# Performance work log

Measured on AMD Instinct MI355X. Metric: run time of the kernel, lower is better.

Reference implementation:

```python
import jax, jax.numpy as jnp
import numpy as np


def _layernorm(x, g, b, eps=1e-5):
    mu = x.mean(-1, keepdims=True)
    var = ((x - mu) ** 2).mean(-1, keepdims=True)
    return (x - mu) / jnp.sqrt(var + eps) * g + b


def _bilinear_sample(feat, coords):
    # feat: (B,C,H,W,D); coords: (B,C,N,2) normalized to [-1,1]
    # torch.grid_sample(mode='bilinear', padding_mode='zeros', align_corners=True)
    B, C, H, W, D = feat.shape
    x = (coords[..., 0] + 1.0) * 0.5 * (W - 1)  # grid x -> width axis
    y = (coords[..., 1] + 1.0) * 0.5 * (H - 1)  # grid y -> height axis
    x0 = jnp.floor(x)
    y0 = jnp.floor(y)
    wx1 = x - x0
    wy1 = y - y0
    bi = jnp.arange(B)[:, None, None]
    ci = jnp.arange(C)[None, :, None]

    def corner(yi, xi, w):
        inb = (xi >= 0) & (xi < W) & (yi >= 0) & (yi < H)
        xc = jnp.clip(xi, 0, W - 1).astype(jnp.int32)
        yc = jnp.clip(yi, 0, H - 1).astype(jnp.int32)
        v = feat[bi, ci, yc, xc]  # (B,C,N,D) gather
        return v * (w * inb)[..., None]

    return (corner(y0, x0, (1 - wy1) * (1 - wx1))
            + corner(y0, x0 + 1, (1 - wy1) * wx1)
            + corner(y0 + 1, x0, wy1 * (1 - wx1))
            + corner(y0 + 1, x0 + 1, wy1 * wx1))


def setup_inputs() -> dict:
    key = jax.random.key(0)
    ks = jax.random.split(key, 12)
    B, C, N, D, H, W = 2, 8, 16384, 256, 64, 64
    s = 1.0 / np.sqrt(D).astype(np.float32)
    return {
        "queries": jax.random.normal(ks[0], (B, N, D), jnp.float32),
        "image_features": jax.random.normal(ks[1], (B, C, H, W, D), jnp.float32),
        "pixel_coords": jax.random.uniform(ks[2], (B, C, N, 2), jnp.float32) * 2.0 - 1.0,
        "valid_mask": jax.random.randint(ks[3], (B, C, N), 0, 2).astype(jnp.int32),
        "Wq": jax.random.normal(ks[4], (D, D), jnp.float32) * s,
        "bq": jnp.zeros((D,), jnp.float32),
        "Wkv": jax.random.normal(ks[5], (D, 2 * D), jnp.float32) * s,
        "bkv": jnp.zeros((2 * D,), jnp.float32),
        "Wo": jax.random.normal(ks[6], (D, D), jnp.float32) * s,
        "bo": jnp.zeros((D,), jnp.float32),
        "gamma": jnp.ones((D,), jnp.float32),
        "beta": jnp.zeros((D,), jnp.float32),
    }


def reference(queries, image_features, pixel_coords, valid_mask,
              Wq, bq, Wkv, bkv, Wo, bo, gamma, beta):
    B, N, D = queries.shape
    residual = queries
    qn = _layernorm(queries, gamma, beta)
    sampled = _bilinear_sample(image_features, pixel_coords)      # (B,C,N,D)
    sampled = jnp.transpose(sampled, (0, 2, 1, 3))                 # (B,N,C,D)
    q = qn @ Wq + bq                                               # (B,N,D)
    kv = sampled @ Wkv + bkv                                       # (B,N,C,2D)
    k, v = kv[..., :D], kv[..., D:]
    scores = jnp.einsum('bnd,bncd->bnc', q, k) / jnp.sqrt(jnp.float32(D))
    valid = jnp.transpose(valid_mask, (0, 2, 1)) != 0              # (B,N,C)
    scores = jnp.where(valid, scores, -jnp.inf)
    attn = jax.nn.softmax(scores, axis=-1)
    attn = jnp.where(jnp.isnan(attn), 0.0, attn)                   # all-invalid -> 0
    out = jnp.einsum('bnc,bncd->bnd', attn, v)
    return residual + out @ Wo + bo
```

## Files before the change

### kernel.cpp

```cpp
#include <hip/hip_runtime.h>
#include <math.h>

#define NROWS 32768

typedef __attribute__((ext_vector_type(8))) short short8;
typedef __attribute__((ext_vector_type(4))) float f32x4;

#define WS_ABF    0
#define WS_WVOBF  32768
#define WS_PB     65536
#define WS_BVO    65792
#define WS_SUMA   66048
#define WS_P      98816
#define WS_FEATBF 8487424

__device__ __forceinline__ unsigned short f2bf(float f) {
    unsigned u = __builtin_bit_cast(unsigned, f);
    u += 0x7FFFu + ((u >> 16) & 1u);
    return (unsigned short)(u >> 16);
}
__device__ __forceinline__ float bf_lo(unsigned u) {
    return __builtin_bit_cast(float, u << 16);
}
__device__ __forceinline__ float bf_hi(unsigned u) {
    return __builtin_bit_cast(float, u & 0xFFFF0000u);
}

__global__ __launch_bounds__(256)
void precompute_kernel(const float* __restrict__ Wq, const float* __restrict__ bq,
                       const float* __restrict__ Wkv, const float* __restrict__ bkv,
                       const float* __restrict__ Wo, const float* __restrict__ feat,
                       float* __restrict__ ws) {
    int t = threadIdx.x;
    int blk = blockIdx.x;
    if (blk >= 514) {
        long i = (long)(blk - 514) * 1024 + t * 4;
        float4 v = *(const float4*)(feat + i);
        unsigned lo = (unsigned)f2bf(v.x) | ((unsigned)f2bf(v.y) << 16);
        unsigned hi = (unsigned)f2bf(v.z) | ((unsigned)f2bf(v.w) << 16);
        *(uint2*)((unsigned short*)(ws + WS_FEATBF) + i) = make_uint2(lo, hi);
        return;
    }
    if (blk < 256) {
        int f = blk;
        const float4* wq4 = (const float4*)(Wq + f * 256);
        const float4* wk4 = (const float4*)(Wkv + (long)t * 512);
        float acc = 0.f;
        #pragma unroll 8
        for (int d4 = 0; d4 < 64; ++d4) {
            float4 a = wq4[d4], b = wk4[d4];
            acc += a.x * b.x + a.y * b.y + a.z * b.z + a.w * b.w;
        }
        ((unsigned short*)(ws + WS_ABF))[t * 256 + f] = f2bf(acc);
    } else if (blk < 512) {
        int e = blk - 256;
        float acc = 0.f;
        for (int g = 0; g < 256; ++g)
            acc = fmaf(Wkv[(long)e * 512 + 256 + g], Wo[g * 256 + t], acc);
        ((unsigned short*)(ws + WS_WVOBF))[t * 256 + e] = f2bf(acc);
    } else if (blk == 512) {
        float acc = 0.f;
        for (int d = 0; d < 256; ++d)
            acc = fmaf(bq[d], Wkv[(long)t * 512 + d], acc);
        ws[WS_PB + t] = acc;
    } else {
        float acc = 0.f;
        for (int g = 0; g < 256; ++g)
            acc = fmaf(bkv[256 + g], Wo[g * 256 + t], acc);
        ws[WS_BVO + t] = acc;
    }
}

__global__ __launch_bounds__(256)
void ln_p_mfma(const float* __restrict__ queries, const float* __restrict__ gamma,
               const float* __restrict__ beta, float* __restrict__ ws) {
    __shared__ unsigned short qs[64][264];
    const unsigned short* Abf = (const unsigned short*)(ws + WS_ABF);
    const float* pb = ws + WS_PB;
    float* pbuf = ws + WS_P;
    int tid = threadIdx.x, wave = tid >> 6, lane = tid & 63;
    long row0 = (long)blockIdx.x * 64;

    float4 g4 = *(const float4*)(gamma + 4 * lane);
    float4 b4 = *(const float4*)(beta + 4 * lane);
    for (int rr = 0; rr < 16; ++rr) {
        int r = wave * 16 + rr;
        float4 v = *(const float4*)(queries + (row0 + r) * 256 + 4 * lane);
        float s = v.x + v.y + v.z + v.w;
        s += __shfl_xor(s, 32); s += __shfl_xor(s, 16); s += __shfl_xor(s, 8);
        s += __shfl_xor(s, 4);  s += __shfl_xor(s, 2);  s += __shfl_xor(s, 1);
        float mu = s * 0.00390625f;
        float dx = v.x - mu, dy = v.y - mu, dz = v.z - mu, dw = v.w - mu;
        float vv = dx * dx + dy * dy + dz * dz + dw * dw;
        vv += __shfl_xor(vv, 32); vv += __shfl_xor(vv, 16); vv += __shfl_xor(vv, 8);
        vv += __shfl_xor(vv, 4);  vv += __shfl_xor(vv, 2);  vv += __shfl_xor(vv, 1);
        float rstd = rsqrtf(vv * 0.00390625f + 1e-5f);
        float qx = dx * rstd * g4.x + b4.x;
        float qy = dy * rstd * g4.y + b4.y;
        float qz = dz * rstd * g4.z + b4.z;
        float qw = dw * rstd * g4.w + b4.w;
        unsigned lo = (unsigned)f2bf(qx) | ((unsigned)f2bf(qy) << 16);
        unsigned hi = (unsigned)f2bf(qz) | ((unsigned)f2bf(qw) << 16);
        *(uint2*)&qs[r][4 * lane] = make_uint2(lo, hi);
    }
    __syncthreads();

    int r16 = lane & 15, g = lane >> 4;
    f32x4 zero = {0.f, 0.f, 0.f, 0.f};
    f32x4 acc[4][4];
    #pragma unroll
    for (int mt = 0; mt < 4; ++mt)
        #pragma unroll
        for (int nt = 0; nt < 4; ++nt) acc[mt][nt] = zero;

    #pragma unroll
    for (int ks = 0; ks < 8; ++ks) {
        short8 bfr[4], afr[4];
        #pragma unroll
        for (int nt = 0; nt < 4; ++nt)
            bfr[nt] = *(const short8*)(Abf + ((wave * 64 + nt * 16 + r16) << 8) + ks * 32 + g * 8);
        #pragma unroll
        for (int mt = 0; mt < 4; ++mt)
            afr[mt] = *(const short8*)(&qs[mt * 16 + r16][ks * 32 + g * 8]);
        #pragma unroll
        for (int mt = 0; mt < 4; ++mt)
            #pragma unroll
            for (int nt = 0; nt < 4; ++nt)
                acc[mt][nt] = __builtin_amdgcn_mfma_f32_16x16x32_bf16(afr[mt], bfr[nt], acc[mt][nt], 0, 0, 0);
    }

    float pbv[4];
    #pragma unroll
    for (int nt = 0; nt < 4; ++nt) pbv[nt] = pb[wave * 64 + nt * 16 + r16];
    #pragma unroll
    for (int mt = 0; mt < 4; ++mt)
        #pragma unroll
        for (int nt = 0; nt < 4; ++nt)
            #pragma unroll
            for (int rg = 0; rg < 4; ++rg)
                pbuf[(row0 + mt * 16 + g * 4 + rg) * 256 + wave * 64 + nt * 16 + r16] =
                    acc[mt][nt][rg] + pbv[nt];
}

__global__ __launch_bounds__(256)
void sample_attn_bf(const float* __restrict__ coords, const int* __restrict__ vmask,
                    float* __restrict__ ws) {
    float* pbuf = ws + WS_P;
    float* suma = ws + WS_SUMA;
    const unsigned short* featbf = (const unsigned short*)(ws + WS_FEATBF);
    int tid = threadIdx.x, wave = tid >> 6, lane = tid & 63;
    long row = (long)blockIdx.x * 4 + wave;
    int b = (int)(row >> 14);
    int n = (int)(row & 16383);

    float4 p4 = *(const float4*)(pbuf + row * 256 + 4 * lane);

    float4 sc[8];
    float score[8];
    bool vld[8];
    #pragma unroll
    for (int c = 0; c < 8; ++c) {
        long cb = (long)(b * 8 + c) * 16384 + n;
        float cx = coords[2 * cb];
        float cy = coords[2 * cb + 1];
        vld[c] = (vmask[cb] != 0);
        float x = (cx + 1.f) * 31.5f;
        float y = (cy + 1.f) * 31.5f;
        float x0f = floorf(x), y0f = floorf(y);
        float wx = x - x0f, wy = y - y0f;
        int ix0 = (int)x0f, iy0 = (int)y0f;
        int ix1 = ix0 + 1, iy1 = iy0 + 1;
        float bx0 = (ix0 >= 0 && ix0 < 64) ? 1.f : 0.f;
        float bx1 = (ix1 >= 0 && ix1 < 64) ? 1.f : 0.f;
        float by0 = (iy0 >= 0 && iy0 < 64) ? 1.f : 0.f;
        float by1 = (iy1 >= 0 && iy1 < 64) ? 1.f : 0.f;
        int cx0 = min(max(ix0, 0), 63), cx1 = min(max(ix1, 0), 63);
        int cy0 = min(max(iy0, 0), 63), cy1 = min(max(iy1, 0), 63);
        const unsigned short* fb = featbf + ((long)(b * 8 + c) << 20);
        const uint2* r00 = (const uint2*)(fb + ((cy0 * 64 + cx0) << 8)) + lane;
        const uint2* r01 = (const uint2*)(fb + ((cy0 * 64 + cx1) << 8)) + lane;
        const uint2* r10 = (const uint2*)(fb + ((cy1 * 64 + cx0) << 8)) + lane;
        const uint2* r11 = (const uint2*)(fb + ((cy1 * 64 + cx1) << 8)) + lane;
        float w00 = (1.f - wy) * (1.f - wx) * by0 * bx0;
        float w01 = (1.f - wy) * wx * by0 * bx1;
        float w10 = wy * (1.f - wx) * by1 * bx0;
        float w11 = wy * wx * by1 * bx1;
        uint2 v00 = *r00, v01 = *r01, v10 = *r10, v11 = *r11;
        float4 s;
        s.x = w00 * bf_lo(v00.x) + w01 * bf_lo(v01.x) + w10 * bf_lo(v10.x) + w11 * bf_lo(v11.x);
        s.y = w00 * bf_hi(v00.x) + w01 * bf_hi(v01.x) + w10 * bf_hi(v10.x) + w11 * bf_hi(v11.x);
        s.z = w00 * bf_lo(v00.y) + w01 * bf_lo(v01.y) + w10 * bf_lo(v10.y) + w11 * bf_lo(v11.y);
        s.w = w00 * bf_hi(v00.y) + w01 * bf_hi(v01.y) + w10 * bf_hi(v10.y) + w11 * bf_hi(v11.y);
        sc[c] = s;
        float t = s.x * p4.x + s.y * p4.y + s.z * p4.z + s.w * p4.w;
        t += __shfl_xor(t, 32); t += __shfl_xor(t, 16); t += __shfl_xor(t, 8);
        t += __shfl_xor(t, 4);  t += __shfl_xor(t, 2);  t += __shfl_xor(t, 1);
        score[c] = t * 0.0625f;
    }

    float m = -INFINITY;
    #pragma unroll
    for (int c = 0; c < 8; ++c) if (vld[c]) m = fmaxf(m, score[c]);
    float4 sb = {0.f, 0.f, 0.f, 0.f};
    float sa = 0.f;
    if (m > -INFINITY) {
        float w[8], s = 0.f;
        #pragma unroll
        for (int c = 0; c < 8; ++c) { w[c] = vld[c] ? expf(score[c] - m) : 0.f; s += w[c]; }
        float inv = 1.f / s;
        #pragma unroll
        for (int c = 0; c < 8; ++c) {
            float a = w[c] * inv;
            sb.x = fmaf(a, sc[c].x, sb.x);
            sb.y = fmaf(a, sc[c].y, sb.y);
            sb.z = fmaf(a, sc[c].z, sb.z);
            sb.w = fmaf(a, sc[c].w, sb.w);
        }
        sa = 1.f;
    }
    unsigned lo = (unsigned)f2bf(sb.x) | ((unsigned)f2bf(sb.y) << 16);
    unsigned hi = (unsigned)f2bf(sb.z) | ((unsigned)f2bf(sb.w) << 16);
    ((uint2*)((char*)pbuf + row * 1024))[lane] = make_uint2(lo, hi);
    if (lane == 0) suma[row] = sa;
}

__global__ __launch_bounds__(256)
void final_mfma(const float* __restrict__ queries, const float* __restrict__ bo,
                const float* __restrict__ ws, float* __restrict__ out) {
    __shared__ unsigned short qs[64][264];
    __shared__ float ssu[64];
    const unsigned short* Wvobf = (const unsigned short*)(ws + WS_WVOBF);
    const float* bvo = ws + WS_BVO;
    const float* suma = ws + WS_SUMA;
    const float* pbuf = ws + WS_P;
    int tid = threadIdx.x, wave = tid >> 6, lane = tid & 63;
    long row0 = (long)blockIdx.x * 64;

    for (int rr = 0; rr < 16; ++rr) {
        int r = wave * 16 + rr;
        uint2 v = ((const uint2*)((const char*)pbuf + (row0 + r) * 1024))[lane];
        *(uint2*)&qs[r][4 * lane] = v;
    }
    if (tid < 64) ssu[tid] = suma[row0 + tid];
    __syncthreads();

    int r16 = lane & 15, g = lane >> 4;
    f32x4 zero = {0.f, 0.f, 0.f, 0.f};
    f32x4 acc[4][4];
    #pragma unroll
    for (int mt = 0; mt < 4; ++mt)
        #pragma unroll
        for (int nt = 0; nt < 4; ++nt) acc[mt][nt] = zero;

    #pragma unroll
    for (int ks = 0; ks < 8; ++ks) {
        short8 bfr[4], afr[4];
        #pragma unroll
        for (int nt = 0; nt < 4; ++nt)
            bfr[nt] = *(const short8*)(Wvobf + ((wave * 64 + nt * 16 + r16) << 8) + ks * 32 + g * 8);
        #pragma unroll
        for (int mt = 0; mt < 4; ++mt)
            afr[mt] = *(const short8*)(&qs[mt * 16 + r16][ks * 32 + g * 8]);
        #pragma unroll
        for (int mt = 0; mt < 4; ++mt)
            #pragma unroll
            for (int nt = 0; nt < 4; ++nt)
                acc[mt][nt] = __builtin_amdgcn_mfma_f32_16x16x32_bf16(afr[mt], bfr[nt], acc[mt][nt], 0, 0, 0);
    }

    float bvov[4], bov[4];
    #pragma unroll
    for (int nt = 0; nt < 4; ++nt) {
        int col = wave * 64 + nt * 16 + r16;
        bvov[nt] = bvo[col];
        bov[nt] = bo[col];
    }
    #pragma unroll
    for (int mt = 0; mt < 4; ++mt)
        #pragma unroll
        for (int nt = 0; nt < 4; ++nt)
            #pragma unroll
            for (int rg = 0; rg < 4; ++rg) {
                long row = row0 + mt * 16 + g * 4 + rg;
                int col = wave * 64 + nt * 16 + r16;
                out[row * 256 + col] = queries[row * 256 + col] + acc[mt][nt][rg]
                                     + ssu[mt * 16 + g * 4 + rg] * bvov[nt] + bov[nt];
            }
}

extern "C" void kernel_launch(void* const* d_in, const int* in_sizes, int n_in,
                              void* d_out, int out_size, void* d_ws, size_t ws_size,
                              hipStream_t stream) {
    const float* queries = (const float*)d_in[0];
    const float* feat    = (const float*)d_in[1];
    const float* coords  = (const float*)d_in[2];
    const int*   vmask   = (const int*)  d_in[3];
    const float* Wq      = (const float*)d_in[4];
    const float* bq      = (const float*)d_in[5];
    const float* Wkv     = (const float*)d_in[6];
    const float* bkv     = (const float*)d_in[7];
    const float* Wo      = (const float*)d_in[8];
    const float* bo      = (const float*)d_in[9];
    const float* gamma   = (const float*)d_in[10];
    const float* beta    = (const float*)d_in[11];
    float* out = (float*)d_out;
    float* ws  = (float*)d_ws;

    precompute_kernel<<<514 + 16384, 256, 0, stream>>>(Wq, bq, Wkv, bkv, Wo, feat, ws);
    ln_p_mfma<<<NROWS / 64, 256, 0, stream>>>(queries, gamma, beta, ws);
    sample_attn_bf<<<NROWS / 4, 256, 0, stream>>>(coords, vmask, ws);
    final_mfma<<<NROWS / 64, 256, 0, stream>>>(queries, bo, ws, out);
}
```

Measured before the change: 278.3 us.

## Store projected queries as bf16, pre-swizzle weights, process two rows per wave

The projected query buffer P is now written as bf16 with the 1/sqrt(D) scale folded in, staged through LDS so global stores are coalesced. This halves P traffic and shrinks the workspace. Weight matrices are stored in MFMA fragment order so each lane's B-fragment load is contiguous. The sampling kernel processes two rows per wave with 16-byte gathers, uses fast exp, and adds unroll pragmas to the small precompute loops. The cost is extra bf16 rounding on the query projection, plus more registers per thread in the sampling kernel.

Measured after the change: 363.9 us. +30.8%, slower.

```diff
diff --git a/kernel.cpp b/kernel.cpp
--- a/kernel.cpp
+++ b/kernel.cpp
@@ -7,12 +7,12 @@
 typedef __attribute__((ext_vector_type(4))) float f32x4;
 
 #define WS_ABF    0
-#define WS_WVOBF  32768
+#define WS_WVOF   32768
 #define WS_PB     65536
 #define WS_BVO    65792
 #define WS_SUMA   66048
 #define WS_P      98816
-#define WS_FEATBF 8487424
+#define WS_FEATBF 4293120
 
 __device__ __forceinline__ unsigned short f2bf(float f) {
     unsigned u = __builtin_bit_cast(unsigned, f);
@@ -24,6 +24,11 @@
 }
 __device__ __forceinline__ float bf_hi(unsigned u) {
     return __builtin_bit_cast(float, u & 0xFFFF0000u);
+}
+__device__ __forceinline__ int fragidx(int outcol, int k) {
+    int ct = outcol >> 4, r16 = outcol & 15;
+    int ks = k >> 5, g = (k >> 3) & 3, j = k & 7;
+    return ((((ct << 3) + ks) << 6) + (g << 4) + r16) * 8 + j;
 }
 
 __global__ __launch_bounds__(256)
@@ -51,20 +56,23 @@
             float4 a = wq4[d4], b = wk4[d4];
             acc += a.x * b.x + a.y * b.y + a.z * b.z + a.w * b.w;
         }
-        ((unsigned short*)(ws + WS_ABF))[t * 256 + f] = f2bf(acc);
+        ((unsigned short*)(ws + WS_ABF))[fragidx(t, f)] = f2bf(acc);
     } else if (blk < 512) {
         int e = blk - 256;
         float acc = 0.f;
+        #pragma unroll 8
         for (int g = 0; g < 256; ++g)
             acc = fmaf(Wkv[(long)e * 512 + 256 + g], Wo[g * 256 + t], acc);
-        ((unsigned short*)(ws + WS_WVOBF))[t * 256 + e] = f2bf(acc);
+        ((unsigned short*)(ws + WS_WVOF))[fragidx(t, e)] = f2bf(acc);
     } else if (blk == 512) {
         float acc = 0.f;
+        #pragma unroll 8
         for (int d = 0; d < 256; ++d)
             acc = fmaf(bq[d], Wkv[(long)t * 512 + d], acc);
         ws[WS_PB + t] = acc;
     } else {
         float acc = 0.f;
+        #pragma unroll 8
         for (int g = 0; g < 256; ++g)
             acc = fmaf(bkv[256 + g], Wo[g * 256 + t], acc);
         ws[WS_BVO + t] = acc;
@@ -75,9 +83,9 @@
 void ln_p_mfma(const float* __restrict__ queries, const float* __restrict__ gamma,
                const float* __restrict__ beta, float* __restrict__ ws) {
     __shared__ unsigned short qs[64][264];
-    const unsigned short* Abf = (const unsigned short*)(ws + WS_ABF);
+    const unsigned short* Afrag = (const unsigned short*)(ws + WS_ABF);
     const float* pb = ws + WS_PB;
-    float* pbuf = ws + WS_P;
+    unsigned short* pbf = (unsigned short*)(ws + WS_P);
     int tid = threadIdx.x, wave = tid >> 6, lane = tid & 63;
     long row0 = (long)blockIdx.x * 64;
 
@@ -118,7 +126,7 @@
         short8 bfr[4], afr[4];
         #pragma unroll
         for (int nt = 0; nt < 4; ++nt)
-            bfr[nt] = *(const short8*)(Abf + ((wave * 64 + nt * 16 + r16) << 8) + ks * 32 + g * 8);
+            bfr[nt] = *(const short8*)(Afrag + (((((wave * 4 + nt) << 3) + ks) << 6) + lane) * 8);
         #pragma unroll
         for (int mt = 0; mt < 4; ++mt)
             afr[mt] = *(const short8*)(&qs[mt * 16 + r16][ks * 32 + g * 8]);
@@ -128,6 +136,7 @@
             for (int nt = 0; nt < 4; ++nt)
                 acc[mt][nt] = __builtin_amdgcn_mfma_f32_16x16x32_bf16(afr[mt], bfr[nt], acc[mt][nt], 0, 0, 0);
     }
+    __syncthreads();
 
     float pbv[4];
     #pragma unroll
@@ -138,34 +147,46 @@
         for (int nt = 0; nt < 4; ++nt)
             #pragma unroll
             for (int rg = 0; rg < 4; ++rg)
-                pbuf[(row0 + mt * 16 + g * 4 + rg) * 256 + wave * 64 + nt * 16 + r16] =
-                    acc[mt][nt][rg] + pbv[nt];
+                qs[mt * 16 + g * 4 + rg][wave * 64 + nt * 16 + r16] =
+                    f2bf((acc[mt][nt][rg] + pbv[nt]) * 0.0625f);
+    __syncthreads();
+
+    for (int rr = 0; rr < 16; ++rr) {
+        int r = wave * 16 + rr;
+        uint2 v = *(const uint2*)&qs[r][4 * lane];
+        *(uint2*)(pbf + ((row0 + r) << 8) + 4 * lane) = v;
+    }
 }
 
 __global__ __launch_bounds__(256)
-void sample_attn_bf(const float* __restrict__ coords, const int* __restrict__ vmask,
-                    float* __restrict__ ws) {
-    float* pbuf = ws + WS_P;
+void sample_attn2(const float* __restrict__ coords, const int* __restrict__ vmask,
+                  float* __restrict__ ws) {
+    unsigned short* pbf = (unsigned short*)(ws + WS_P);
     float* suma = ws + WS_SUMA;
     const unsigned short* featbf = (const unsigned short*)(ws + WS_FEATBF);
     int tid = threadIdx.x, wave = tid >> 6, lane = tid & 63;
-    long row = (long)blockIdx.x * 4 + wave;
+    int h = lane >> 5, l5 = lane & 31;
+    long row = (long)blockIdx.x * 8 + wave * 2 + h;
     int b = (int)(row >> 14);
     int n = (int)(row & 16383);
 
-    float4 p4 = *(const float4*)(pbuf + row * 256 + 4 * lane);
-
-    float4 sc[8];
+    uint4 pv = *(const uint4*)(pbf + (row << 8) + (l5 << 3));
+    float p8[8];
+    p8[0] = bf_lo(pv.x); p8[1] = bf_hi(pv.x);
+    p8[2] = bf_lo(pv.y); p8[3] = bf_hi(pv.y);
+    p8[4] = bf_lo(pv.z); p8[5] = bf_hi(pv.z);
+    p8[6] = bf_lo(pv.w); p8[7] = bf_hi(pv.w);
+
+    float sc[8][8];
     float score[8];
     bool vld[8];
     #pragma unroll
     for (int c = 0; c < 8; ++c) {
-        long cb = (long)(b * 8 + c) * 16384 + n;
-        float cx = coords[2 * cb];
-        float cy = coords[2 * cb + 1];
+        long cb = ((long)(b * 8 + c) << 14) + n;
+        float2 cxy = *(const float2*)(coords + 2 * cb);
         vld[c] = (vmask[cb] != 0);
-        float x = (cx + 1.f) * 31.5f;
-        float y = (cy + 1.f) * 31.5f;
+        float x = (cxy.x + 1.f) * 31.5f;
+        float y = (cxy.y + 1.f) * 31.5f;
         float x0f = floorf(x), y0f = floorf(y);
         float wx = x - x0f, wy = y - y0f;
         int ix0 = (int)x0f, iy0 = (int)y0f;
@@ -177,51 +198,59 @@
         int cx0 = min(max(ix0, 0), 63), cx1 = min(max(ix1, 0), 63);
         int cy0 = min(max(iy0, 0), 63), cy1 = min(max(iy1, 0), 63);
         const unsigned short* fb = featbf + ((long)(b * 8 + c) << 20);
-        const uint2* r00 = (const uint2*)(fb + ((cy0 * 64 + cx0) << 8)) + lane;
-        const uint2* r01 = (const uint2*)(fb + ((cy0 * 64 + cx1) << 8)) + lane;
-        const uint2* r10 = (const uint2*)(fb + ((cy1 * 64 + cx0) << 8)) + lane;
-        const uint2* r11 = (const uint2*)(fb + ((cy1 * 64 + cx1) << 8)) + lane;
         float w00 = (1.f - wy) * (1.f - wx) * by0 * bx0;
         float w01 = (1.f - wy) * wx * by0 * bx1;
         float w10 = wy * (1.f - wx) * by1 * bx0;
         float w11 = wy * wx * by1 * bx1;
-        uint2 v00 = *r00, v01 = *r01, v10 = *r10, v11 = *r11;
-        float4 s;
-        s.x = w00 * bf_lo(v00.x) + w01 * bf_lo(v01.x) + w10 * bf_lo(v10.x) + w11 * bf_lo(v11.x);
-        s.y = w00 * bf_hi(v00.x) + w01 * bf_hi(v01.x) + w10 * bf_hi(v10.x) + w11 * bf_hi(v11.x);
-        s.z = w00 * bf_lo(v00.y) + w01 * bf_lo(v01.y) + w10 * bf_lo(v10.y) + w11 * bf_lo(v11.y);
-        s.w = w00 * bf_hi(v00.y) + w01 * bf_hi(v01.y) + w10 * bf_hi(v10.y) + w11 * bf_hi(v11.y);
-        sc[c] = s;
-        float t = s.x * p4.x + s.y * p4.y + s.z * p4.z + s.w * p4.w;
-        t += __shfl_xor(t, 32); t += __shfl_xor(t, 16); t += __shfl_xor(t, 8);
+        uint4 v00 = *(const uint4*)(fb + ((cy0 * 64 + cx0) << 8) + (l5 << 3));
+        uint4 v01 = *(const uint4*)(fb + ((cy0 * 64 + cx1) << 8) + (l5 << 3));
+        uint4 v10 = *(const uint4*)(fb + ((cy1 * 64 + cx0) << 8) + (l5 << 3));
+        uint4 v11 = *(const uint4*)(fb + ((cy1 * 64 + cx1) << 8) + (l5 << 3));
+        float t0 = 0.f, t1 = 0.f;
+        #pragma unroll
+        for (int j = 0; j < 4; ++j) {
+            unsigned u00 = (&v00.x)[j], u01 = (&v01.x)[j], u10 = (&v10.x)[j], u11 = (&v11.x)[j];
+            float e0 = w00 * bf_lo(u00) + w01 * bf_lo(u01) + w10 * bf_lo(u10) + w11 * bf_lo(u11);
+            float e1 = w00 * bf_hi(u00) + w01 * bf_hi(u01) + w10 * bf_hi(u10) + w11 * bf_hi(u11);
+            sc[c][2 * j] = e0;
+            sc[c][2 * j + 1] = e1;
+            t0 = fmaf(e0, p8[2 * j], t0);
+            t1 = fmaf(e1, p8[2 * j + 1], t1);
+        }
+        float t = t0 + t1;
+        t += __shfl_xor(t, 16); t += __shfl_xor(t, 8);
         t += __shfl_xor(t, 4);  t += __shfl_xor(t, 2);  t += __shfl_xor(t, 1);
-        score[c] = t * 0.0625f;
+        score[c] = t;
     }
 
     float m = -INFINITY;
     #pragma unroll
     for (int c = 0; c < 8; ++c) if (vld[c]) m = fmaxf(m, score[c]);
-    float4 sb = {0.f, 0.f, 0.f, 0.f};
+    float o8[8];
+    #pragma unroll
+    for (int j = 0; j < 8; ++j) o8[j] = 0.f;
     float sa = 0.f;
     if (m > -INFINITY) {
         float w[8], s = 0.f;
         #pragma unroll
-        for (int c = 0; c < 8; ++c) { w[c] = vld[c] ? expf(score[c] - m) : 0.f; s += w[c]; }
+        for (int c = 0; c < 8; ++c) { w[c] = vld[c] ? __expf(score[c] - m) : 0.f; s += w[c]; }
         float inv = 1.f / s;
         #pragma unroll
         for (int c = 0; c < 8; ++c) {
             float a = w[c] * inv;
-            sb.x = fmaf(a, sc[c].x, sb.x);
-            sb.y = fmaf(a, sc[c].y, sb.y);
-            sb.z = fmaf(a, sc[c].z, sb.z);
-            sb.w = fmaf(a, sc[c].w, sb.w);
+            #pragma unroll
+            for (int j = 0; j < 8; ++j)
+                o8[j] = fmaf(a, sc[c][j], o8[j]);
         }
         sa = 1.f;
     }
-    unsigned lo = (unsigned)f2bf(sb.x) | ((unsigned)f2bf(sb.y) << 16);
-    unsigned hi = (unsigned)f2bf(sb.z) | ((unsigned)f2bf(sb.w) << 16);
-    ((uint2*)((char*)pbuf + row * 1024))[lane] = make_uint2(lo, hi);
-    if (lane == 0) suma[row] = sa;
+    uint4 pk;
+    pk.x = (unsigned)f2bf(o8[0]) | ((unsigned)f2bf(o8[1]) << 16);
+    pk.y = (unsigned)f2bf(o8[2]) | ((unsigned)f2bf(o8[3]) << 16);
+    pk.z = (unsigned)f2bf(o8[4]) | ((unsigned)f2bf(o8[5]) << 16);
+    pk.w = (unsigned)f2bf(o8[6]) | ((unsigned)f2bf(o8[7]) << 16);
+    *(uint4*)(pbf + (row << 8) + (l5 << 3)) = pk;
+    if (l5 == 0) suma[row] = sa;
 }
 
 __global__ __launch_bounds__(256)
@@ -229,16 +258,16 @@
                 const float* __restrict__ ws, float* __restrict__ out) {
     __shared__ unsigned short qs[64][264];
     __shared__ float ssu[64];
-    const unsigned short* Wvobf = (const unsigned short*)(ws + WS_WVOBF);
+    const unsigned short* Wfrag = (const unsigned short*)(ws + WS_WVOF);
     const float* bvo = ws + WS_BVO;
     const float* suma = ws + WS_SUMA;
-    const float* pbuf = ws + WS_P;
+    const unsigned short* pbf = (const unsigned short*)(ws + WS_P);
     int tid = threadIdx.x, wave = tid >> 6, lane = tid & 63;
     long row0 = (long)blockIdx.x * 64;
 
     for (int rr = 0; rr < 16; ++rr) {
         int r = wave * 16 + rr;
-        uint2 v = ((const uint2*)((const char*)pbuf + (row0 + r) * 1024))[lane];
+        uint2 v = *(const uint2*)(pbf + ((row0 + r) << 8) + 4 * lane);
         *(uint2*)&qs[r][4 * lane] = v;
     }
     if (tid < 64) ssu[tid] = suma[row0 + tid];
@@ -257,7 +286,7 @@
         short8 bfr[4], afr[4];
         #pragma unroll
         for (int nt = 0; nt < 4; ++nt)
-            bfr[nt] = *(const short8*)(Wvobf + ((wave * 64 + nt * 16 + r16) << 8) + ks * 32 + g * 8);
+            bfr[nt] = *(const short8*)(Wfrag + (((((wave * 4 + nt) << 3) + ks) << 6) + lane) * 8);
         #pragma unroll
         for (int mt = 0; mt < 4; ++mt)
             afr[mt] = *(const short8*)(&qs[mt * 16 + r16][ks * 32 + g * 8]);
@@ -308,6 +337,6 @@
 
     precompute_kernel<<<514 + 16384, 256, 0, stream>>>(Wq, bq, Wkv, bkv, Wo, feat, ws);
     ln_p_mfma<<<NROWS / 64, 256, 0, stream>>>(queries, gamma, beta, ws);
-    sample_attn_bf<<<NROWS / 4, 256, 0, stream>>>(coords, vmask, ws);
+    sample_attn2<<<NROWS / 8, 256, 0, stream>>>(coords, vmask, ws);
     final_mfma<<<NROWS / 64, 256, 0, stream>>>(queries, bo, ws, out);
 }
```
